# Optimization experiments

Hardware: AMD Instinct MI355X
Metric: run time of the kernel (lower is better)

The kernel has to match this reference:

```python
import jax, jax.numpy as jnp
import numpy as np

LEAK = 0.9  # leaky-integrator rate of the ESN cell


def setup_inputs() -> dict:
    key = jax.random.key(0)
    ks = jax.random.split(key, 7)
    S, B, I, R = 512, 64, 256, 2048
    sc_in0 = 1.0 / np.sqrt(I)
    sc_h = 0.9 / np.sqrt(R)  # ~spectral-radius style scaling
    sc_in1 = 1.0 / np.sqrt(R)
    return {
        "x": jax.random.normal(ks[0], (S, B, I), jnp.float32),
        "W_in0": jax.random.normal(ks[1], (R, I), jnp.float32) * sc_in0,
        "W_hh0": jax.random.normal(ks[2], (R, R), jnp.float32) * sc_h,
        "b0": jax.random.normal(ks[3], (R,), jnp.float32) * 0.1,
        "W_in1": jax.random.normal(ks[4], (R, R), jnp.float32) * sc_in1,
        "W_hh1": jax.random.normal(ks[5], (R, R), jnp.float32) * sc_h,
        "b1": jax.random.normal(ks[6], (R,), jnp.float32) * 0.1,
    }


def _esn_layer(x_seq, W_in, W_hh, b):
    # x_seq: (S, B, D_in); returns (S, B, R), (B, R)
    B = x_seq.shape[1]
    R = W_hh.shape[0]
    h0 = jnp.zeros((B, R), x_seq.dtype)
    # Precompute input projection for all timesteps in one big GEMM.
    xin = jnp.einsum('sbd,rd->sbr', x_seq, W_in) + b

    def step(h, xin_t):
        h_new = (1.0 - LEAK) * h + LEAK * jnp.tanh(xin_t + h @ W_hh.T)
        return h_new, h_new

    h_n, ys = jax.lax.scan(step, h0, xin)
    return ys, h_n


def reference(x, W_in0, W_hh0, b0, W_in1, W_hh1, b1):
    y0, h0n = _esn_layer(x, W_in0, W_hh0, b0)
    y1, h1n = _esn_layer(y0, W_in1, W_hh1, b1)
    h_n = jnp.stack([h0n, h1n])  # (num_layers, B, R)
    return y1, h_n
```

## Files before the change

### kernel.cpp

```cpp
#include <hip/hip_runtime.h>

typedef _Float16 half8 __attribute__((ext_vector_type(8)));
typedef float floatx4 __attribute__((ext_vector_type(4)));

#define S_LEN 512
#define NB 64
#define NI 256
#define NR 2048
#define LEAK 0.9f

#define NBLK 256
#define TPB 512
#define NBNR ((size_t)NB * NR)

#define OFF_BAR ((size_t)0)
#define OFF_H0  ((size_t)4096)
#define OFF_H1  (OFF_H0 + 2 * NBNR * 2)
#define OFF_XE  (OFF_H1 + 2 * NBNR * 2)

__device__ __forceinline__ half8 cvt8(const float* s) {
    float4 p = *(const float4*)s, q = *(const float4*)(s + 4);
    half8 v;
    v[0] = (_Float16)p.x; v[1] = (_Float16)p.y; v[2] = (_Float16)p.z; v[3] = (_Float16)p.w;
    v[4] = (_Float16)q.x; v[5] = (_Float16)q.y; v[6] = (_Float16)q.z; v[7] = (_Float16)q.w;
    return v;
}

__global__ void xprep_kernel(const float* __restrict__ x, _Float16* __restrict__ xe) {
    const int t = blockIdx.x;
    #pragma unroll
    for (int it = 0; it < 4; ++it) {
        const int u = it * 8 + (threadIdx.x >> 6);
        const int l = threadIdx.x & 63;
        const int b = (u >> 3) * 16 + (l & 15);
        const int i0 = (u & 7) * 32 + (l >> 4) * 8;
        half8 v = cvt8(x + ((size_t)t * NB + b) * NI + i0);
        *(half8*)(xe + (size_t)t * NB * NI + (size_t)u * 512 + (size_t)l * 8) = v;
    }
}

__device__ __forceinline__ void stH(_Float16* p, _Float16 v) {
    unsigned short b;
    __builtin_memcpy(&b, &v, 2);
    __hip_atomic_store((unsigned short*)p, b, __ATOMIC_RELAXED, __HIP_MEMORY_SCOPE_AGENT);
}

__device__ __forceinline__ void gbar(unsigned* bar) {
    __syncthreads();
    if (threadIdx.x == 0) {
        unsigned* cnt  = bar + (blockIdx.x & 7) * 32;
        unsigned* root = bar + 256;
        unsigned* gen  = bar + 272;
        unsigned g = __hip_atomic_load(gen, __ATOMIC_RELAXED, __HIP_MEMORY_SCOPE_AGENT);
        bool last = false;
        if (__hip_atomic_fetch_add(cnt, 1u, __ATOMIC_RELAXED, __HIP_MEMORY_SCOPE_AGENT) == (NBLK / 8 - 1)) {
            __hip_atomic_store(cnt, 0u, __ATOMIC_RELAXED, __HIP_MEMORY_SCOPE_AGENT);
            if (__hip_atomic_fetch_add(root, 1u, __ATOMIC_ACQ_REL, __HIP_MEMORY_SCOPE_AGENT) == 7u) {
                __hip_atomic_store(root, 0u, __ATOMIC_RELAXED, __HIP_MEMORY_SCOPE_AGENT);
                __hip_atomic_store(gen, g + 1u, __ATOMIC_RELEASE, __HIP_MEMORY_SCOPE_AGENT);
                last = true;
            }
        }
        if (!last)
            while (__hip_atomic_load(gen, __ATOMIC_RELAXED, __HIP_MEMORY_SCOPE_AGENT) == g)
                __builtin_amdgcn_s_sleep(2);
    }
    __syncthreads();
    __builtin_amdgcn_fence(__ATOMIC_ACQUIRE, "agent");
}

template <int CH, int KU, int ROLE>
__device__ __forceinline__ void esn_layer_run(
    const float* __restrict__ bias_v,
    const float* Whh, const float* Win,
    const char* __restrict__ xe,
    char* hp,
    const char* h0p,
    float* __restrict__ out,
    unsigned* __restrict__ bar,
    float* __restrict__ rsc, int r0, int bhalf)
{
    const int tid = threadIdx.x;
    const int l = tid & 63, w = tid >> 6, l15 = l & 15, g = l >> 4;

    half8 bwA[CH], bwB[CH];
    #pragma unroll
    for (int j = 0; j < CH; ++j) {
        const float* s0; int rs;
        if (j < 8) { s0 = Whh + (size_t)(r0 + l15) * NR + (w * 8 + j) * 32 + g * 8; rs = NR; }
        else if (ROLE == 0) { s0 = Win + (size_t)(r0 + l15) * KU + w * 32 + g * 8; rs = KU; }
        else { s0 = Win + (size_t)(r0 + l15) * KU + (w * 8 + j - 8) * 32 + g * 8; rs = KU; }
        bwA[j] = cvt8(s0);
        bwB[j] = cvt8(s0 + (size_t)16 * rs);
        asm volatile("" : "+v"(bwA[j]));
        asm volatile("" : "+v"(bwB[j]));
    }

    const int fg_o = w & 1, bt_o = (w >> 1) & 1;
    const bool owner = (w < 4);
    const int ncol = r0 + fg_o * 16 + l15;
    const float bias = owner ? bias_v[ncol] : 0.f;
    const int cu = ncol >> 5, gg = (ncol >> 3) & 3, ee = ncol & 7;
    float hs[4] = {0.f, 0.f, 0.f, 0.f};
    float* hn_base = out + (size_t)S_LEN * NBNR + (size_t)ROLE * NBNR;

    for (int s = 0; s < S_LEN + 1; ++s) {
        const int t = (ROLE == 0) ? s : s - 1;
        const bool active = (ROLE == 0) ? (s < S_LEN) : (s >= 1);
        if (active) {
            const char* hu = hp + (size_t)(t & 1) * (NBNR * 2);
            const char* uu = (ROLE == 0) ? xe + (size_t)t * NB * NI * 2
                                         : h0p + (size_t)((t + 1) & 1) * (NBNR * 2);

            floatx4 acc[2][2];
            #pragma unroll
            for (int fg = 0; fg < 2; ++fg)
                #pragma unroll
                for (int bt = 0; bt < 2; ++bt)
                    acc[fg][bt] = (floatx4){0.f, 0.f, 0.f, 0.f};

            #pragma unroll
            for (int bt = 0; bt < 2; ++bt) {
                const int bt_g = bhalf * 2 + bt;
                #pragma unroll
                for (int hv = 0; hv < (CH + 7) / 8; ++hv) {
                    const int jn = (hv == 0) ? ((CH < 8) ? CH : 8) : (CH - 8);
                    half8 abuf[8];
                    #pragma unroll
                    for (int jj = 0; jj < 8; ++jj) {
                        if (jj >= jn) break;
                        const int j = hv * 8 + jj;
                        const char* src; size_t unit;
                        if (j < 8)          { src = hu; unit = (size_t)(bt_g * 64 + w * 8 + j); }
                        else if (ROLE == 0) { src = uu; unit = (size_t)(bt_g * 8 + w); }
                        else                { src = uu; unit = (size_t)(bt_g * 64 + w * 8 + j - 8); }
                        abuf[jj] = *(const half8*)(src + unit * 1024 + (size_t)l * 16);
                    }
                    #pragma unroll
                    for (int jj = 0; jj < 8; ++jj) {
                        if (jj >= jn) break;
                        const int j = hv * 8 + jj;
                        acc[0][bt] = __builtin_amdgcn_mfma_f32_16x16x32_f16(abuf[jj], bwA[j], acc[0][bt], 0, 0, 0);
                        acc[1][bt] = __builtin_amdgcn_mfma_f32_16x16x32_f16(abuf[jj], bwB[j], acc[1][bt], 0, 0, 0);
                    }
                }
            }

            #pragma unroll
            for (int fg = 0; fg < 2; ++fg)
                #pragma unroll
                for (int bt = 0; bt < 2; ++bt)
                    *(floatx4*)(rsc + (size_t)((w * 4 + bt * 2 + fg) * 64 + l) * 4) = acc[fg][bt];
            __syncthreads();

            if (owner) {
                floatx4 r = {0.f, 0.f, 0.f, 0.f};
                #pragma unroll
                for (int v = 0; v < 8; ++v)
                    r += *(const floatx4*)(rsc + (size_t)((v * 4 + w) * 64 + l) * 4);

                char* hw = hp + (size_t)((t + 1) & 1) * (NBNR * 2);
                #pragma unroll
                for (int j = 0; j < 4; ++j) {
                    float hn = (1.0f - LEAK) * hs[j] + LEAK * tanhf(r[j] + bias);
                    hs[j] = hn;
                    const int bj = bhalf * 32 + bt_o * 16 + g * 4 + j;
                    size_t byte = (size_t)((bj >> 4) * 64 + cu) * 1024
                                + (size_t)((gg * 16 + (bj & 15)) * 8 + ee) * 2;
                    stH((_Float16*)(hw + byte), (_Float16)hn);
                    if (ROLE == 1)
                        __builtin_nontemporal_store(hn, out + (size_t)t * NBNR + (size_t)bj * NR + ncol);
                    if (t == S_LEN - 1)
                        __builtin_nontemporal_store(hn, hn_base + (size_t)bj * NR + ncol);
                }
            }
        }
        if (s < S_LEN) gbar(bar);
    }
}

__global__ void __launch_bounds__(TPB, 1) esn_kernel(
    const float* __restrict__ b0v, const float* __restrict__ b1v,
    const float* Whh0, const float* Win0,
    const float* Whh1, const float* Win1,
    const char* __restrict__ xe,
    char* h0p, char* h1p,
    unsigned* __restrict__ bar, float* __restrict__ out)
{
    __shared__ __align__(16) float rsc[32 * 64 * 4];
    const int bid = blockIdx.x;
    const int sub = bid & 127;
    const int r0 = (sub >> 1) * 32;
    const int bhalf = sub & 1;
    if (bid < 128)
        esn_layer_run<9, NI, 0>(b0v, Whh0, Win0, xe, h0p, nullptr,
                                out, bar, rsc, r0, bhalf);
    else
        esn_layer_run<16, NR, 1>(b1v, Whh1, Win1, nullptr, h1p, h0p,
                                 out, bar, rsc, r0, bhalf);
}

extern "C" void kernel_launch(void* const* d_in, const int* in_sizes, int n_in,
                              void* d_out, int out_size, void* d_ws, size_t ws_size,
                              hipStream_t stream) {
    const float* x    = (const float*)d_in[0];
    const float* Win0 = (const float*)d_in[1];
    const float* Whh0 = (const float*)d_in[2];
    const float* b0   = (const float*)d_in[3];
    const float* Win1 = (const float*)d_in[4];
    const float* Whh1 = (const float*)d_in[5];
    const float* b1   = (const float*)d_in[6];

    char* ws = (char*)d_ws;
    char* xe  = ws + OFF_XE;
    char* h0p = ws + OFF_H0;
    char* h1p = ws + OFF_H1;
    unsigned* bar = (unsigned*)(ws + OFF_BAR);
    float* out = (float*)d_out;

    (void)hipMemsetAsync(ws, 0, OFF_XE, stream);

    xprep_kernel<<<dim3(S_LEN), dim3(512), 0, stream>>>(x, (_Float16*)xe);

    void* args[] = { (void*)&b0, (void*)&b1, (void*)&Whh0, (void*)&Win0,
                     (void*)&Whh1, (void*)&Win1, (void*)&xe, (void*)&h0p,
                     (void*)&h1p, (void*)&bar, (void*)&out };
    hipError_t e = hipLaunchCooperativeKernel((void*)esn_kernel, dim3(NBLK), dim3(TPB),
                                              args, 0, stream);
    if (e != hipSuccess) {
        esn_kernel<<<dim3(NBLK), dim3(TPB), 0, stream>>>(
            b0, b1, Whh0, Win0, Whh1, Win1, xe, h0p, h1p, bar, out);
    }
}
```

Baseline: 10.86 ms.

## Move half of resident weight fragments from registers into LDS

Keeps only the first 16-row weight fragment set in VGPRs and stores the second half of each block's weight slice in 128 KB of LDS, reloading it every timestep. The MFMA loop now loads both batch tiles' activations together and reads the LDS weights once per k-chunk. The cross-wave reduction is split into two phases with extra barriers so the scratch buffer can be halved. This is meant to relieve register pressure or spilling from holding 2*CH half8 weight fragments. In exchange it adds LDS reads per step and two more __syncthreads per timestep.

```diff
diff --git a/kernel.cpp b/kernel.cpp
--- a/kernel.cpp
+++ b/kernel.cpp
@@ -78,23 +78,30 @@
     const char* h0p,
     float* __restrict__ out,
     unsigned* __restrict__ bar,
-    float* __restrict__ rsc, int r0, int bhalf)
+    char* wlds, float* rsc, int r0, int bhalf)
 {
     const int tid = threadIdx.x;
     const int l = tid & 63, w = tid >> 6, l15 = l & 15, g = l >> 4;
 
-    half8 bwA[CH], bwB[CH];
+    half8 bwA[CH];
     #pragma unroll
     for (int j = 0; j < CH; ++j) {
-        const float* s0; int rs;
-        if (j < 8) { s0 = Whh + (size_t)(r0 + l15) * NR + (w * 8 + j) * 32 + g * 8; rs = NR; }
-        else if (ROLE == 0) { s0 = Win + (size_t)(r0 + l15) * KU + w * 32 + g * 8; rs = KU; }
-        else { s0 = Win + (size_t)(r0 + l15) * KU + (w * 8 + j - 8) * 32 + g * 8; rs = KU; }
+        const float* s0;
+        if (j < 8)          s0 = Whh + (size_t)(r0 + l15) * NR + (w * 8 + j) * 32 + g * 8;
+        else if (ROLE == 0) s0 = Win + (size_t)(r0 + l15) * KU + w * 32 + g * 8;
+        else                s0 = Win + (size_t)(r0 + l15) * KU + (w * 8 + j - 8) * 32 + g * 8;
         bwA[j] = cvt8(s0);
-        bwB[j] = cvt8(s0 + (size_t)16 * rs);
         asm volatile("" : "+v"(bwA[j]));
-        asm volatile("" : "+v"(bwB[j]));
-    }
+    }
+    #pragma unroll
+    for (int j = 0; j < CH; ++j) {
+        const float* s1;
+        if (j < 8)          s1 = Whh + (size_t)(r0 + 16 + l15) * NR + (w * 8 + j) * 32 + g * 8;
+        else if (ROLE == 0) s1 = Win + (size_t)(r0 + 16 + l15) * KU + w * 32 + g * 8;
+        else                s1 = Win + (size_t)(r0 + 16 + l15) * KU + (w * 8 + j - 8) * 32 + g * 8;
+        *(half8*)(wlds + ((size_t)(w * CH + j) << 10) + (size_t)l * 16) = cvt8(s1);
+    }
+    __syncthreads();
 
     const int fg_o = w & 1, bt_o = (w >> 1) & 1;
     const bool owner = (w < 4);
@@ -111,54 +118,62 @@
             const char* hu = hp + (size_t)(t & 1) * (NBNR * 2);
             const char* uu = (ROLE == 0) ? xe + (size_t)t * NB * NI * 2
                                          : h0p + (size_t)((t + 1) & 1) * (NBNR * 2);
-
-            floatx4 acc[2][2];
+            const int bt_g0 = bhalf * 2, bt_g1 = bhalf * 2 + 1;
+
+            floatx4 c00 = {0,0,0,0}, c01 = {0,0,0,0}, c10 = {0,0,0,0}, c11 = {0,0,0,0};
+
             #pragma unroll
-            for (int fg = 0; fg < 2; ++fg)
-                #pragma unroll
-                for (int bt = 0; bt < 2; ++bt)
-                    acc[fg][bt] = (floatx4){0.f, 0.f, 0.f, 0.f};
-
-            #pragma unroll
-            for (int bt = 0; bt < 2; ++bt) {
-                const int bt_g = bhalf * 2 + bt;
-                #pragma unroll
-                for (int hv = 0; hv < (CH + 7) / 8; ++hv) {
-                    const int jn = (hv == 0) ? ((CH < 8) ? CH : 8) : (CH - 8);
-                    half8 abuf[8];
-                    #pragma unroll
-                    for (int jj = 0; jj < 8; ++jj) {
-                        if (jj >= jn) break;
-                        const int j = hv * 8 + jj;
-                        const char* src; size_t unit;
-                        if (j < 8)          { src = hu; unit = (size_t)(bt_g * 64 + w * 8 + j); }
-                        else if (ROLE == 0) { src = uu; unit = (size_t)(bt_g * 8 + w); }
-                        else                { src = uu; unit = (size_t)(bt_g * 64 + w * 8 + j - 8); }
-                        abuf[jj] = *(const half8*)(src + unit * 1024 + (size_t)l * 16);
-                    }
-                    #pragma unroll
-                    for (int jj = 0; jj < 8; ++jj) {
-                        if (jj >= jn) break;
-                        const int j = hv * 8 + jj;
-                        acc[0][bt] = __builtin_amdgcn_mfma_f32_16x16x32_f16(abuf[jj], bwA[j], acc[0][bt], 0, 0, 0);
-                        acc[1][bt] = __builtin_amdgcn_mfma_f32_16x16x32_f16(abuf[jj], bwB[j], acc[1][bt], 0, 0, 0);
-                    }
-                }
-            }
-
-            #pragma unroll
-            for (int fg = 0; fg < 2; ++fg)
-                #pragma unroll
-                for (int bt = 0; bt < 2; ++bt)
-                    *(floatx4*)(rsc + (size_t)((w * 4 + bt * 2 + fg) * 64 + l) * 4) = acc[fg][bt];
+            for (int hv = 0; hv < (CH + 7) / 8; ++hv) {
+                const int jn = (hv == 0) ? ((CH < 8) ? CH : 8) : (CH - 8);
+                half8 a0[8], a1[8], wb[8];
+                #pragma unroll
+                for (int jj = 0; jj < 8; ++jj) {
+                    if (jj >= jn) break;
+                    const int j = hv * 8 + jj;
+                    const char* src; size_t u0, u1;
+                    if (j < 8)          { src = hu; u0 = (size_t)(bt_g0 * 64 + w * 8 + j);  u1 = (size_t)(bt_g1 * 64 + w * 8 + j); }
+                    else if (ROLE == 0) { src = uu; u0 = (size_t)(bt_g0 * 8 + w);           u1 = (size_t)(bt_g1 * 8 + w); }
+                    else                { src = uu; u0 = (size_t)(bt_g0 * 64 + w * 8 + j - 8); u1 = (size_t)(bt_g1 * 64 + w * 8 + j - 8); }
+                    a0[jj] = *(const half8*)(src + u0 * 1024 + (size_t)l * 16);
+                    a1[jj] = *(const half8*)(src + u1 * 1024 + (size_t)l * 16);
+                }
+                #pragma unroll
+                for (int jj = 0; jj < 8; ++jj) {
+                    if (jj >= jn) break;
+                    const int j = hv * 8 + jj;
+                    wb[jj] = *(const half8*)(wlds + ((size_t)(w * CH + j) << 10) + (size_t)l * 16);
+                }
+                #pragma unroll
+                for (int jj = 0; jj < 8; ++jj) {
+                    if (jj >= jn) break;
+                    const int j = hv * 8 + jj;
+                    c00 = __builtin_amdgcn_mfma_f32_16x16x32_f16(a0[jj], bwA[j], c00, 0, 0, 0);
+                    c01 = __builtin_amdgcn_mfma_f32_16x16x32_f16(a1[jj], bwA[j], c01, 0, 0, 0);
+                    c10 = __builtin_amdgcn_mfma_f32_16x16x32_f16(a0[jj], wb[jj], c10, 0, 0, 0);
+                    c11 = __builtin_amdgcn_mfma_f32_16x16x32_f16(a1[jj], wb[jj], c11, 0, 0, 0);
+                }
+            }
+
+            floatx4 r = {0.f, 0.f, 0.f, 0.f};
+            *(floatx4*)(rsc + (size_t)((w * 2 + 0) * 64 + l) * 4) = c00;
+            *(floatx4*)(rsc + (size_t)((w * 2 + 1) * 64 + l) * 4) = c01;
             __syncthreads();
+            if (owner && (w & 1) == 0) {
+                #pragma unroll
+                for (int v = 0; v < 8; ++v)
+                    r += *(const floatx4*)(rsc + (size_t)((v * 2 + bt_o) * 64 + l) * 4);
+            }
+            __syncthreads();
+            *(floatx4*)(rsc + (size_t)((w * 2 + 0) * 64 + l) * 4) = c10;
+            *(floatx4*)(rsc + (size_t)((w * 2 + 1) * 64 + l) * 4) = c11;
+            __syncthreads();
+            if (owner && (w & 1) == 1) {
+                #pragma unroll
+                for (int v = 0; v < 8; ++v)
+                    r += *(const floatx4*)(rsc + (size_t)((v * 2 + bt_o) * 64 + l) * 4);
+            }
 
             if (owner) {
-                floatx4 r = {0.f, 0.f, 0.f, 0.f};
-                #pragma unroll
-                for (int v = 0; v < 8; ++v)
-                    r += *(const floatx4*)(rsc + (size_t)((v * 4 + w) * 64 + l) * 4);
-
                 char* hw = hp + (size_t)((t + 1) & 1) * (NBNR * 2);
                 #pragma unroll
                 for (int j = 0; j < 4; ++j) {
@@ -187,17 +202,18 @@
     char* h0p, char* h1p,
     unsigned* __restrict__ bar, float* __restrict__ out)
 {
-    __shared__ __align__(16) float rsc[32 * 64 * 4];
+    __shared__ __align__(16) char wlds[128 * 1024];
+    __shared__ __align__(16) float rsc[16 * 64 * 4];
     const int bid = blockIdx.x;
     const int sub = bid & 127;
     const int r0 = (sub >> 1) * 32;
     const int bhalf = sub & 1;
     if (bid < 128)
         esn_layer_run<9, NI, 0>(b0v, Whh0, Win0, xe, h0p, nullptr,
-                                out, bar, rsc, r0, bhalf);
+                                out, bar, wlds, rsc, r0, bhalf);
     else
         esn_layer_run<16, NR, 1>(b1v, Whh1, Win1, nullptr, h1p, h0p,
-                                 out, bar, rsc, r0, bhalf);
+                                 out, bar, wlds, rsc, r0, bhalf);
 }
 
 extern "C" void kernel_launch(void* const* d_in, const int* in_sizes, int n_in,
```

Result: no change. 10.88 ms (+0.2%).
